# Optimization experiments

Measured on AMD Instinct MI355X. Metric: run time of the kernel, lower is better.

Reference implementation:

```python
import jax, jax.numpy as jnp
import numpy as np


def setup_inputs() -> dict:
    key = jax.random.key(0)
    k1, k2, k3 = jax.random.split(key, 3)
    B, Cin, H, W = 64, 16, 256, 256
    Cout, K = 64, 3
    x = jax.random.normal(k1, (B, Cin, H, W), dtype=jnp.float32)
    # PyTorch Conv2d init scale ~ 1/sqrt(fan_in)
    fan_in = Cin * K * K
    conv_weight = jax.random.normal(k2, (Cout, Cin, K, K), dtype=jnp.float32) / np.sqrt(fan_in)
    conv_bias = jax.random.normal(k3, (Cout,), dtype=jnp.float32) / np.sqrt(fan_in)
    return {"x": x, "conv_weight": conv_weight, "conv_bias": conv_bias}


def reference(x, conv_weight, conv_bias):
    # Conv2d: stride=1, padding=0 (VALID), dilation=1, groups=1
    y = jax.lax.conv_general_dilated(
        x, conv_weight,
        window_strides=(1, 1),
        padding="VALID",
        dimension_numbers=("NCHW", "OIHW", "NCHW"),
    ) + conv_bias[None, :, None, None]          # [B, Cout, 254, 254]
    m = jnp.min(y, axis=1, keepdims=True)        # [B, 1, 254, 254] min over channels
    return jnp.tanh(jnp.tanh(m))                 # double tanh
```

## Files before the change

### kernel.cpp

```cpp
#include <hip/hip_runtime.h>
#include <math.h>

#define CIN   16
#define COUT  64
#define H     256
#define W     256
#define OH    254
#define OW    254
#define NTAP  9
#define HWSZ  (H * W)
#define RING  18
#define SROW  136

typedef _Float16 f16x8  __attribute__((ext_vector_type(8)));
typedef float    f32x16 __attribute__((ext_vector_type(16)));

#define BARRIER()                                                               \
    __builtin_amdgcn_sched_barrier(0);                                          \
    asm volatile("s_waitcnt lgkmcnt(0)" ::: "memory");                          \
    __builtin_amdgcn_s_barrier();                                               \
    __builtin_amdgcn_sched_barrier(0);

__global__ void wpack_kernel(const float* __restrict__ w, _Float16* __restrict__ wpk) {
    int idx = blockIdx.x * 256 + threadIdx.x;
    if (idx >= NTAP * 2 * 64 * 8) return;
    int e = idx & 7, l = (idx >> 3) & 63, m = (idx >> 9) & 1, t = idx >> 10;
    int co  = (l & 31) + 32 * m;
    int cin = 8 * (l >> 5) + e;
    wpk[idx] = (_Float16)w[((co * CIN + cin) * 3 + t / 3) * 3 + (t % 3)];
}

__device__ __forceinline__ float tanh_fast(float v) {
    float e = __expf(2.0f * v);
    return 1.0f - 2.0f * __builtin_amdgcn_rcpf(e + 1.0f);
}
__device__ __forceinline__ float min3f(float a, float b, float c) {
    return fminf(fminf(a, b), c);
}

__global__ __launch_bounds__(256, 2) void conv_mfma_kernel(
        const float* __restrict__ x, const f16x8* __restrict__ wpk,
        const float* __restrict__ bias, float* __restrict__ out) {
    __shared__ f16x8 ring[RING * SROW];
    __shared__ float bias_lds[64];

    const int tid  = threadIdx.x;
    const int lane = tid & 63;

    int bid = blockIdx.x;
    int nb  = (bid & 7) * 64 + (bid >> 3);
    const int img  = nb >> 3;
    const int rem  = nb & 7;
    const int colb = rem & 3;
    const int half = rem >> 2;
    const int base = 64 * colb;
    const int R0   = 128 * half;
    const int S0   = half ? 2 : 0;

    const float* xb = x + (size_t)img * CIN * HWSZ;

    f16x8 wreg[NTAP][2];
#pragma unroll
    for (int t = 0; t < NTAP; ++t)
#pragma unroll
        for (int m = 0; m < 2; ++m)
            wreg[t][m] = wpk[(t * 2 + m) * 64 + lane];

    if (tid < 64) {
        int q = tid & 15, m = (tid >> 4) & 1, g = tid >> 5;
        bias_lds[tid] = bias[(q & 3) + 8 * (q >> 2) + 4 * g + 32 * m];
    }

    int r8[3], gq[3], gx[3], wof[3];
#pragma unroll
    for (int k = 0; k < 3; ++k) {
        int u  = tid + 256 * k;
        r8[k]  = u / 68;
        int r2 = u - 68 * r8[k];
        int g  = (r2 >= 34) ? 1 : 0;
        int p  = r2 - 34 * g;
        int px = base + 2 * p; if (px > 254) px = 254;
        gq[k]  = g;
        gx[k]  = px;
        wof[k] = g * 68 + 2 * p;
    }
    const bool act2 = (tid < 32);

    float2 vA[8], vB[8], vC[8];

#define PLOADK(k, rowAbs, vv)                                                   \
    {                                                                           \
        int gr = (rowAbs); if (gr > 255) gr = 255;                              \
        const float* gp = xb + (size_t)(8 * gq[k]) * HWSZ + (size_t)gr * W + gx[k]; \
        _Pragma("unroll")                                                       \
        for (int cc = 0; cc < 8; ++cc) vv[cc] = *(const float2*)(gp + (size_t)cc * HWSZ); \
    }

#define PWRITEK(k, slot, vv)                                                    \
    {                                                                           \
        f16x8 q0, q1;                                                           \
        _Pragma("unroll")                                                       \
        for (int cc = 0; cc < 8; ++cc) { q0[cc] = (_Float16)vv[cc].x;           \
                                         q1[cc] = (_Float16)vv[cc].y; }         \
        const int ad = (slot) * SROW + wof[k];                                  \
        ring[ad]     = q0;                                                      \
        ring[ad + 1] = q1;                                                      \
    }

#pragma unroll
    for (int k = 0; k < 3; ++k) {
        int u = tid + 256 * k;
        if (k == 2 && tid >= 168) break;
        int r10 = u / 68;
        int r2  = u - 68 * r10;
        int g   = (r2 >= 34) ? 1 : 0;
        int p   = r2 - 34 * g;
        int px  = base + 2 * p; if (px > 254) px = 254;
        const float* gp = xb + (size_t)(8 * g) * HWSZ + (size_t)(R0 + r10) * W + px;
        float2 vm[8];
#pragma unroll
        for (int cc = 0; cc < 8; ++cc) vm[cc] = *(const float2*)(gp + (size_t)cc * HWSZ);
        f16x8 q0, q1;
#pragma unroll
        for (int cc = 0; cc < 8; ++cc) { q0[cc] = (_Float16)vm[cc].x;
                                         q1[cc] = (_Float16)vm[cc].y; }
        const int ad = (S0 + r10) * SROW + g * 68 + 2 * p;
        ring[ad]     = q0;
        ring[ad + 1] = q1;
    }

    PLOADK(0, R0 + 10 + r8[0], vA)
    PLOADK(1, R0 + 10 + r8[1], vB)
    if (act2) PLOADK(2, R0 + 10 + r8[2], vC)
    BARRIER()

    const int wv  = tid >> 6;
    const int s   = wv & 1;
    const int rg  = wv >> 1;
    const int l31 = lane & 31;
    const int g2  = lane >> 5;
    const int foff = g2 * 68 + 32 * s + l31;
    const int opx  = base + 32 * s + l31;
    const size_t obase = (size_t)img * OH * OW;
    const f32x16* bp = (const f32x16*)(bias_lds + g2 * 32);

    int slot0 = S0;

#pragma unroll 1
    for (int t = 0; t < 16; ++t) {
        const int row0 = R0 + 8 * t;

#pragma unroll
        for (int c = 0; c < 2; ++c) {
            const int rowoff = 4 * rg + 2 * c;
            f32x16 cb0 = bp[0], cb1 = bp[1];
            f32x16 acc[2][2];
#pragma unroll
            for (int dd = 0; dd < 4; ++dd) {
                int sl = slot0 + rowoff + dd; if (sl >= RING) sl -= RING;
                const f16x8* rp = ring + sl * SROW + foff;
                f16x8 f0 = rp[0], f1 = rp[1], f2 = rp[2];
#pragma unroll
                for (int kw = 0; kw < 3; ++kw) {
                    f16x8 ff = (kw == 0) ? f0 : (kw == 1) ? f1 : f2;
#pragma unroll
                    for (int ro = 0; ro < 2; ++ro) {
                        const int kh = dd - ro;
                        if (kh < 0 || kh > 2) continue;
#pragma unroll
                        for (int m = 0; m < 2; ++m) {
                            const f32x16& cin_ = (kh == 0 && kw == 0)
                                               ? (m == 0 ? cb0 : cb1) : acc[ro][m];
                            acc[ro][m] = __builtin_amdgcn_mfma_f32_32x32x16_f16(
                                wreg[kh * 3 + kw][m], ff, cin_, 0, 0, 0);
                        }
                    }
                }
            }
#pragma unroll
            for (int ro = 0; ro < 2; ++ro) {
                float mn = fminf(acc[ro][0][0], acc[ro][1][0]);
#pragma unroll
                for (int q = 1; q < 16; ++q)
                    mn = min3f(acc[ro][0][q], acc[ro][1][q], mn);
                mn = fminf(mn, __shfl_xor(mn, 32));
                float t2 = tanh_fast(tanh_fast(mn));
                const int oh = row0 + rowoff + ro;
                if (g2 == 0 && oh < OH && opx < OW)
                    out[obase + (size_t)oh * OW + opx] = t2;
            }
        }

        if (t <= 14) {
            int sl0 = slot0 + 10 + r8[0]; if (sl0 >= RING) sl0 -= RING;
            int sl1 = slot0 + 10 + r8[1]; if (sl1 >= RING) sl1 -= RING;
            PWRITEK(0, sl0, vA)
            PWRITEK(1, sl1, vB)
            if (act2) {
                int sl2 = slot0 + 10 + r8[2]; if (sl2 >= RING) sl2 -= RING;
                PWRITEK(2, sl2, vC)
            }
        }
        if (t <= 13) {
            PLOADK(0, row0 + 18 + r8[0], vA)
            PLOADK(1, row0 + 18 + r8[1], vB)
            if (act2) PLOADK(2, row0 + 18 + r8[2], vC)
        }
        BARRIER()
        slot0 += 8; if (slot0 >= RING) slot0 -= RING;
    }
}

extern "C" void kernel_launch(void* const* d_in, const int* in_sizes, int n_in,
                              void* d_out, int out_size, void* d_ws, size_t ws_size,
                              hipStream_t stream) {
    const float* x    = (const float*)d_in[0];
    const float* w    = (const float*)d_in[1];
    const float* bias = (const float*)d_in[2];
    float* out = (float*)d_out;
    _Float16* wpk = (_Float16*)d_ws;

    wpack_kernel<<<36, 256, 0, stream>>>(w, wpk);
    conv_mfma_kernel<<<512, 256, 0, stream>>>(x, (const f16x8*)wpk, bias, out);
}
```

Measured before the change: 91.13 us.

## Shrink LDS ring to 14 rows with 4-row steps and double-buffered prefetch

Restructures the row pipeline so each block iteration computes 4 output rows instead of 8. It uses a 14-slot LDS ring indexed by row modulo, and alternates two register prefetch buffers that load rows 8 ahead. This cuts LDS usage, which could allow more resident blocks, and shortens the per-stage critical section. The cost is twice as many barriers, modulo arithmetic for slot indices, and extra registers for the doubled prefetch buffers. The last iterations also issue extra clamped loads.

```diff
diff --git a/kernel.cpp b/kernel.cpp
--- a/kernel.cpp
+++ b/kernel.cpp
@@ -9,7 +9,7 @@
 #define OW    254
 #define NTAP  9
 #define HWSZ  (H * W)
-#define RING  18
+#define RING  14
 #define SROW  136
 
 typedef _Float16 f16x8  __attribute__((ext_vector_type(8)));
@@ -55,7 +55,6 @@
     const int half = rem >> 2;
     const int base = 64 * colb;
     const int R0   = 128 * half;
-    const int S0   = half ? 2 : 0;
 
     const float* xb = x + (size_t)img * CIN * HWSZ;
 
@@ -71,12 +70,12 @@
         bias_lds[tid] = bias[(q & 3) + 8 * (q >> 2) + 4 * g + 32 * m];
     }
 
-    int r8[3], gq[3], gx[3], wof[3];
-#pragma unroll
-    for (int k = 0; k < 3; ++k) {
+    int r4[2], gq[2], gx[2], wof[2];
+#pragma unroll
+    for (int k = 0; k < 2; ++k) {
         int u  = tid + 256 * k;
-        r8[k]  = u / 68;
-        int r2 = u - 68 * r8[k];
+        r4[k]  = u / 68;
+        int r2 = u - 68 * r4[k];
         int g  = (r2 >= 34) ? 1 : 0;
         int p  = r2 - 34 * g;
         int px = base + 2 * p; if (px > 254) px = 254;
@@ -84,9 +83,9 @@
         gx[k]  = px;
         wof[k] = g * 68 + 2 * p;
     }
-    const bool act2 = (tid < 32);
-
-    float2 vA[8], vB[8], vC[8];
+    const bool act1 = (tid < 16);
+
+    float2 vA0[8], vA1[8], vB0[8], vB1[8];
 
 #define PLOADK(k, rowAbs, vv)                                                   \
     {                                                                           \
@@ -106,6 +105,8 @@
         ring[ad]     = q0;                                                      \
         ring[ad + 1] = q1;                                                      \
     }
+
+#define SLOT(rowAbs) ((rowAbs) % RING)
 
 #pragma unroll
     for (int k = 0; k < 3; ++k) {
@@ -124,14 +125,15 @@
 #pragma unroll
         for (int cc = 0; cc < 8; ++cc) { q0[cc] = (_Float16)vm[cc].x;
                                          q1[cc] = (_Float16)vm[cc].y; }
-        const int ad = (S0 + r10) * SROW + g * 68 + 2 * p;
+        const int ad = SLOT(R0 + r10) * SROW + g * 68 + 2 * p;
         ring[ad]     = q0;
         ring[ad + 1] = q1;
     }
 
-    PLOADK(0, R0 + 10 + r8[0], vA)
-    PLOADK(1, R0 + 10 + r8[1], vB)
-    if (act2) PLOADK(2, R0 + 10 + r8[2], vC)
+    PLOADK(0, R0 + 10 + r4[0], vA0)
+    if (act1) PLOADK(1, R0 + 10 + r4[1], vA1)
+    PLOADK(0, R0 + 14 + r4[0], vB0)
+    if (act1) PLOADK(1, R0 + 14 + r4[1], vB1)
     BARRIER()
 
     const int wv  = tid >> 6;
@@ -144,70 +146,68 @@
     const size_t obase = (size_t)img * OH * OW;
     const f32x16* bp = (const f32x16*)(bias_lds + g2 * 32);
 
-    int slot0 = S0;
+#define COMPUTE_TILE(t)                                                         \
+    {                                                                           \
+        const int row0 = R0 + 4 * (t);                                          \
+        const int rowoff = 2 * rg;                                              \
+        f32x16 cb0 = bp[0], cb1 = bp[1];                                        \
+        f32x16 acc[2][2];                                                       \
+        _Pragma("unroll")                                                       \
+        for (int dd = 0; dd < 4; ++dd) {                                        \
+            const f16x8* rp = ring + SLOT(row0 + rowoff + dd) * SROW + foff;    \
+            f16x8 f0 = rp[0], f1 = rp[1], f2 = rp[2];                           \
+            _Pragma("unroll")                                                   \
+            for (int kw = 0; kw < 3; ++kw) {                                    \
+                f16x8 ff = (kw == 0) ? f0 : (kw == 1) ? f1 : f2;                \
+                _Pragma("unroll")                                               \
+                for (int ro = 0; ro < 2; ++ro) {                                \
+                    const int kh = dd - ro;                                     \
+                    if (kh < 0 || kh > 2) continue;                             \
+                    _Pragma("unroll")                                           \
+                    for (int m = 0; m < 2; ++m) {                               \
+                        const f32x16& ci = (kh == 0 && kw == 0)                 \
+                                         ? (m == 0 ? cb0 : cb1) : acc[ro][m];   \
+                        acc[ro][m] = __builtin_amdgcn_mfma_f32_32x32x16_f16(    \
+                            wreg[kh * 3 + kw][m], ff, ci, 0, 0, 0);             \
+                    }                                                           \
+                }                                                               \
+            }                                                                   \
+        }                                                                       \
+        _Pragma("unroll")                                                       \
+        for (int ro = 0; ro < 2; ++ro) {                                        \
+            float mn = fminf(acc[ro][0][0], acc[ro][1][0]);                     \
+            _Pragma("unroll")                                                   \
+            for (int q = 1; q < 16; ++q)                                        \
+                mn = min3f(acc[ro][0][q], acc[ro][1][q], mn);                   \
+            mn = fminf(mn, __shfl_xor(mn, 32));                                 \
+            float t2 = tanh_fast(tanh_fast(mn));                                \
+            const int oh = row0 + rowoff + ro;                                  \
+            if (g2 == 0 && oh < OH && opx < OW)                                 \
+                out[obase + (size_t)oh * OW + opx] = t2;                        \
+        }                                                                       \
+    }
 
 #pragma unroll 1
-    for (int t = 0; t < 16; ++t) {
-        const int row0 = R0 + 8 * t;
-
-#pragma unroll
-        for (int c = 0; c < 2; ++c) {
-            const int rowoff = 4 * rg + 2 * c;
-            f32x16 cb0 = bp[0], cb1 = bp[1];
-            f32x16 acc[2][2];
-#pragma unroll
-            for (int dd = 0; dd < 4; ++dd) {
-                int sl = slot0 + rowoff + dd; if (sl >= RING) sl -= RING;
-                const f16x8* rp = ring + sl * SROW + foff;
-                f16x8 f0 = rp[0], f1 = rp[1], f2 = rp[2];
-#pragma unroll
-                for (int kw = 0; kw < 3; ++kw) {
-                    f16x8 ff = (kw == 0) ? f0 : (kw == 1) ? f1 : f2;
-#pragma unroll
-                    for (int ro = 0; ro < 2; ++ro) {
-                        const int kh = dd - ro;
-                        if (kh < 0 || kh > 2) continue;
-#pragma unroll
-                        for (int m = 0; m < 2; ++m) {
-                            const f32x16& cin_ = (kh == 0 && kw == 0)
-                                               ? (m == 0 ? cb0 : cb1) : acc[ro][m];
-                            acc[ro][m] = __builtin_amdgcn_mfma_f32_32x32x16_f16(
-                                wreg[kh * 3 + kw][m], ff, cin_, 0, 0, 0);
-                        }
-                    }
-                }
-            }
-#pragma unroll
-            for (int ro = 0; ro < 2; ++ro) {
-                float mn = fminf(acc[ro][0][0], acc[ro][1][0]);
-#pragma unroll
-                for (int q = 1; q < 16; ++q)
-                    mn = min3f(acc[ro][0][q], acc[ro][1][q], mn);
-                mn = fminf(mn, __shfl_xor(mn, 32));
-                float t2 = tanh_fast(tanh_fast(mn));
-                const int oh = row0 + rowoff + ro;
-                if (g2 == 0 && oh < OH && opx < OW)
-                    out[obase + (size_t)oh * OW + opx] = t2;
-            }
-        }
-
-        if (t <= 14) {
-            int sl0 = slot0 + 10 + r8[0]; if (sl0 >= RING) sl0 -= RING;
-            int sl1 = slot0 + 10 + r8[1]; if (sl1 >= RING) sl1 -= RING;
-            PWRITEK(0, sl0, vA)
-            PWRITEK(1, sl1, vB)
-            if (act2) {
-                int sl2 = slot0 + 10 + r8[2]; if (sl2 >= RING) sl2 -= RING;
-                PWRITEK(2, sl2, vC)
-            }
-        }
-        if (t <= 13) {
-            PLOADK(0, row0 + 18 + r8[0], vA)
-            PLOADK(1, row0 + 18 + r8[1], vB)
-            if (act2) PLOADK(2, row0 + 18 + r8[2], vC)
+    for (int j = 0; j < 16; ++j) {
+        const int t0 = 2 * j, t1 = 2 * j + 1;
+        COMPUTE_TILE(t0)
+        {
+            const int wr = R0 + 4 * t0 + 10;
+            PWRITEK(0, SLOT(wr + r4[0]), vA0)
+            if (act1) PWRITEK(1, SLOT(wr + r4[1]), vA1)
+            PLOADK(0, wr + 8 + r4[0], vA0)
+            if (act1) PLOADK(1, wr + 8 + r4[1], vA1)
         }
         BARRIER()
-        slot0 += 8; if (slot0 >= RING) slot0 -= RING;
+        COMPUTE_TILE(t1)
+        {
+            const int wr = R0 + 4 * t1 + 10;
+            PWRITEK(0, SLOT(wr + r4[0]), vB0)
+            if (act1) PWRITEK(1, SLOT(wr + r4[1]), vB1)
+            PLOADK(0, wr + 8 + r4[0], vB0)
+            if (act1) PLOADK(1, wr + 8 + r4[1], vB1)
+        }
+        BARRIER()
     }
 }
 
```

New measurement: 92.91 us. About the same (+2.0%).
